# Performance work log

Hardware: AMD Instinct MI355X
Metric: run time of the kernel (lower is better)

The kernel has to match this reference:

```python
import jax, jax.numpy as jnp
import numpy as np

EMB_DIM = 1024
N_HEADS = 16  # per-head feature size after the module's axis-swapped split
D_HEAD = EMB_DIM // N_HEADS  # 64, acts as the number of attention groups
BATCH = 2
SEQ = 1024


def setup_inputs() -> dict:
    key = jax.random.key(0)
    ks = jax.random.split(key, 5)
    s = 0.02
    return {
        "x": jax.random.normal(ks[0], (BATCH, SEQ, EMB_DIM), dtype=jnp.float32),
        "Wq": jax.random.normal(ks[1], (EMB_DIM, EMB_DIM), dtype=jnp.float32) * s,
        "Wk": jax.random.normal(ks[2], (EMB_DIM, EMB_DIM), dtype=jnp.float32) * s,
        "Wv": jax.random.normal(ks[3], (EMB_DIM, EMB_DIM), dtype=jnp.float32) * s,
        "Wo": jax.random.normal(ks[4], (EMB_DIM, EMB_DIM), dtype=jnp.float32) * s,
        "bo": jnp.zeros((EMB_DIM,), dtype=jnp.float32),
    }


def reference(x, Wq, Wk, Wv, Wo, bo):
    b, n, d = x.shape
    q = x @ Wq  # [b, n, d]
    k = x @ Wk
    v = x @ Wv

    # Faithful to original split(): view (b, n, d_head, n_heads) then swap -> (b, d_head, n, n_heads)
    def split(t):
        return t.reshape(b, n, D_HEAD, N_HEADS).transpose(0, 2, 1, 3)

    q, k, v = split(q), split(k), split(v)  # [b, D_HEAD, n, N_HEADS]

    scores = jnp.einsum("bhqe,bhke->bhqk", q, k)  # [b, D_HEAD, n, n]
    causal = jnp.triu(jnp.ones((n, n), dtype=bool), k=1)
    scores = jnp.where(causal, -jnp.inf, scores)
    # Original scales by sqrt(q.shape[-1]) == sqrt(N_HEADS)
    attn = jax.nn.softmax(scores / jnp.sqrt(jnp.float32(N_HEADS)), axis=-1)
    # dropout p=0.0 (eval) -> identity
    ctx = jnp.einsum("bhqk,bhke->bhqe", attn, v)  # [b, D_HEAD, n, N_HEADS]
    ctx = ctx.transpose(0, 2, 1, 3).reshape(b, n, d)  # [b, n, emb_dim]
    return ctx @ Wo + bo
```

## Files before the change

### kernel.cpp

```cpp
#include <hip/hip_runtime.h>
#include <hip/hip_bf16.h>
#include <stdint.h>

typedef __bf16 bf16;
typedef __attribute__((ext_vector_type(8))) __bf16 bf16x8;
typedef __attribute__((ext_vector_type(4))) __bf16 bf16x4;
typedef __attribute__((ext_vector_type(2))) __bf16 bf16x2;
typedef __attribute__((ext_vector_type(4))) float f32x4;
typedef __attribute__((ext_vector_type(16))) float f32x16;
typedef __attribute__((ext_vector_type(4))) uint32_t u32x4;
typedef __attribute__((ext_vector_type(2))) uint32_t u32x2;

#define CSL 0.36067376022224085f

__device__ __forceinline__ f32x4 mfma_16x16x32(bf16x8 a, bf16x8 b, f32x4 c) {
    return __builtin_amdgcn_mfma_f32_16x16x32_bf16(a, b, c, 0, 0, 0);
}
__device__ __forceinline__ f32x16 mfma_32x32x16(bf16x8 a, bf16x8 b, f32x16 c) {
    return __builtin_amdgcn_mfma_f32_32x32x16_bf16(a, b, c, 0, 0, 0);
}

__device__ __forceinline__ void gload_lds16(const void* g, void* l) {
    __builtin_amdgcn_global_load_lds((const __attribute__((address_space(1))) uint32_t*)g,
                                     (__attribute__((address_space(3))) uint32_t*)l, 16, 0, 0);
}

__device__ __forceinline__ uint32_t cvtpk_bf16(float lo, float hi) {
    uint32_t r;
    asm("v_cvt_pk_bf16_f32 %0, %1, %2" : "=v"(r) : "v"(lo), "v"(hi));
    return r;
}
__device__ __forceinline__ u32x2 pl32(uint32_t a, uint32_t b) {
    return __builtin_amdgcn_permlane32_swap(a, b, false, false);
}
__device__ __forceinline__ bf16x8 mk_frag(uint32_t a, uint32_t b, uint32_t c, uint32_t d) {
    u32x4 t; t[0] = a; t[1] = b; t[2] = c; t[3] = d;
    return __builtin_bit_cast(bf16x8, t);
}

__global__ __launch_bounds__(256) void convert_x(const float* __restrict__ x,
                                                 bf16* __restrict__ xb) {
    const int i = blockIdx.x * 256 + threadIdx.x;
    const float4 v = ((const float4*)x)[i];
    bf16x4 o;
    o[0] = (bf16)v.x; o[1] = (bf16)v.y; o[2] = (bf16)v.z; o[3] = (bf16)v.w;
    ((bf16x4*)xb)[i] = o;
}

__global__ __launch_bounds__(256) void transcvt(const float* __restrict__ w0,
                                                const float* __restrict__ w1,
                                                const float* __restrict__ w2,
                                                const float* __restrict__ w3,
                                                bf16* __restrict__ o0,
                                                bf16* __restrict__ o1,
                                                bf16* __restrict__ o2,
                                                bf16* __restrict__ o3) {
    __shared__ float t[32][33];
    const float* src;
    bf16* dst;
    switch (blockIdx.z) {
        case 0: src = w0; dst = o0; break;
        case 1: src = w1; dst = o1; break;
        case 2: src = w2; dst = o2; break;
        default: src = w3; dst = o3; break;
    }
    const int tx = threadIdx.x, ty = threadIdx.y;
    const int bx = blockIdx.x * 32, by = blockIdx.y * 32;
#pragma unroll
    for (int i = 0; i < 4; ++i)
        t[ty + i * 8][tx] = src[(size_t)(by + ty + i * 8) * 1024 + bx + tx];
    __syncthreads();
#pragma unroll
    for (int i = 0; i < 4; ++i)
        dst[(size_t)(bx + ty + i * 8) * 1024 + by + tx] = (bf16)t[tx][ty + i * 8];
}

template<int NCOLS, int OUTF32>
__global__ __launch_bounds__(256) void gemm_bt(const bf16* __restrict__ A,
                                               const bf16* __restrict__ Bt,
                                               void* __restrict__ Cout,
                                               const float* __restrict__ bias) {
    __shared__ __align__(16) bf16 As[4096];
    __shared__ __align__(16) bf16 Bs[4096];
    const int tid = threadIdx.x;
    const int l = tid & 63, w = tid >> 6;
    const int hi = l >> 4, lo = l & 15;
    const int wr = w >> 1, wc = w & 1;
    const int brow = blockIdx.y * 128;
    const int bcol = blockIdx.x * 128;

    f32x4 acc[4][4] = {};

    for (int ks = 0; ks < 32; ++ks) {
        __syncthreads();
#pragma unroll
        for (int rnd = 0; rnd < 2; ++rnd) {
            const int u = tid + rnd * 256;
            const int kc = u >> 7, row = u & 127;
            gload_lds16(A  + (size_t)(brow + row) * 1024 + ks * 32 + kc * 8, As + u * 8);
            gload_lds16(Bt + (size_t)(bcol + row) * 1024 + ks * 32 + kc * 8, Bs + u * 8);
        }
        __syncthreads();
        bf16x8 af[4], bfr[4];
#pragma unroll
        for (int m = 0; m < 4; ++m)
            af[m] = *(const bf16x8*)(As + (hi * 128 + wr * 64 + m * 16 + lo) * 8);
#pragma unroll
        for (int n = 0; n < 4; ++n)
            bfr[n] = *(const bf16x8*)(Bs + (hi * 128 + wc * 64 + n * 16 + lo) * 8);
#pragma unroll
        for (int m = 0; m < 4; ++m)
#pragma unroll
            for (int n = 0; n < 4; ++n)
                acc[m][n] = mfma_16x16x32(af[m], bfr[n], acc[m][n]);
    }

#pragma unroll
    for (int m = 0; m < 4; ++m) {
        const int row0 = brow + wr * 64 + m * 16 + hi * 4;
#pragma unroll
        for (int n = 0; n < 4; ++n) {
            const int col = bcol + wc * 64 + n * 16 + lo;
            if (OUTF32) {
                float* C = (float*)Cout;
                const float bv = bias[col];
#pragma unroll
                for (int r = 0; r < 4; ++r)
                    C[(size_t)(row0 + r) * NCOLS + col] = acc[m][n][r] + bv;
            } else {
                bf16* C = (bf16*)Cout;
#pragma unroll
                for (int r = 0; r < 4; ++r)
                    C[(size_t)(row0 + r) * NCOLS + col] = (bf16)acc[m][n][r];
            }
        }
    }
}

__global__ __launch_bounds__(256) void attn_kernel(const bf16* __restrict__ qkv,
                                                   bf16* __restrict__ ctx) {
    __shared__ __align__(16) bf16 VT[16][1032];
    __shared__ __align__(16) bf16 KS[1024 * 16];
    const int h = blockIdx.y, bb = blockIdx.z;
    const int tid = threadIdx.x;
    const int w = tid >> 6, l = tid & 63;
    const int l5 = l & 31, hi2 = l >> 5;
    const bf16* base = qkv + (size_t)bb * 1024 * 3072;

#pragma unroll
    for (int it = 0; it < 4; ++it) {
        const int kv = it * 256 + tid;
        const bf16* vp = base + (size_t)kv * 3072 + 2048 + h * 16;
        bf16x8 v0 = *(const bf16x8*)(vp);
        bf16x8 v1 = *(const bf16x8*)(vp + 8);
#pragma unroll
        for (int e = 0; e < 8; ++e) { VT[e][kv] = v0[e]; VT[e + 8][kv] = v1[e]; }
        const bf16* kp = base + (size_t)kv * 3072 + 1024 + h * 16;
        bf16x8 k0 = *(const bf16x8*)(kp);
        bf16x8 k1 = *(const bf16x8*)(kp + 8);
        const int swz = ((kv >> 2) & 1) << 4;
        char* krow = (char*)KS + kv * 32;
        *(bf16x8*)(krow + (0 ^ swz))  = k0;
        *(bf16x8*)(krow + (16 ^ swz)) = k1;
    }
    __syncthreads();

    const int p = blockIdx.x * 4 + w;
    const int qts[2] = {p, 31 - p};

#pragma unroll 1
    for (int t = 0; t < 2; ++t) {
        const int qt = qts[t];
        const int qg = qt * 32 + l5;

        const bf16x8 qf = *(const bf16x8*)(base + (size_t)qg * 3072 + h * 16 + hi2 * 8);

        f32x16 accA = {}, accB = {};
        const f32x16 zero = {};
        float s_own = 0.0f;

        const int kv0 = l5;
        bf16x8 kf = *(const bf16x8*)((const char*)KS + kv0 * 32 +
                                     ((hi2 << 4) ^ (((kv0 >> 2) & 1) << 4)));
        bf16x8 v1f = *(const bf16x8*)(&VT[l & 15][hi2 * 8]);
        bf16x8 v2f = *(const bf16x8*)(&VT[l & 15][16 + hi2 * 8]);

        for (int kt = 0; kt <= qt; ++kt) {
            const bf16x8 kfc = kf, v1c = v1f, v2c = v2f;
            if (kt < qt) {
                const int kvn = (kt + 1) * 32 + l5;
                kf  = *(const bf16x8*)((const char*)KS + kvn * 32 +
                                       ((hi2 << 4) ^ (((kvn >> 2) & 1) << 4)));
                v1f = *(const bf16x8*)(&VT[l & 15][(kt + 1) * 32 + hi2 * 8]);
                v2f = *(const bf16x8*)(&VT[l & 15][(kt + 1) * 32 + 16 + hi2 * 8]);
            }
            const f32x16 st = mfma_32x32x16(kfc, qf, zero);

            f32x16 pr;
            if (kt < qt) {
#pragma unroll
                for (int r = 0; r < 16; ++r) pr[r] = exp2f(st[r] * CSL);
            } else {
                const int lim = qg - kt * 32;
#pragma unroll
                for (int r = 0; r < 16; ++r) {
                    const int kvr = (r & 3) + 8 * (r >> 2) + 4 * hi2;
                    pr[r] = (kvr <= lim) ? exp2f(st[r] * CSL) : 0.0f;
                }
            }
            const float b0 = (pr[0] + pr[1]) + (pr[2] + pr[3]);
            const float b1 = (pr[4] + pr[5]) + (pr[6] + pr[7]);
            const float b2 = (pr[8] + pr[9]) + (pr[10] + pr[11]);
            const float b3 = (pr[12] + pr[13]) + (pr[14] + pr[15]);
            s_own += (b0 + b1) + (b2 + b3);

            const uint32_t wa1 = cvtpk_bf16(pr[0], pr[1]), wb1 = cvtpk_bf16(pr[2], pr[3]);
            const uint32_t wc1 = cvtpk_bf16(pr[4], pr[5]), wd1 = cvtpk_bf16(pr[6], pr[7]);
            const u32x2 sA = pl32(wa1, wc1), sB = pl32(wb1, wd1);
            const bf16x8 pf1 = mk_frag(sA.x, sB.x, sA.y, sB.y);
            const uint32_t wa2 = cvtpk_bf16(pr[8], pr[9]),   wb2 = cvtpk_bf16(pr[10], pr[11]);
            const uint32_t wc2 = cvtpk_bf16(pr[12], pr[13]), wd2 = cvtpk_bf16(pr[14], pr[15]);
            const u32x2 sC = pl32(wa2, wc2), sD = pl32(wb2, wd2);
            const bf16x8 pf2 = mk_frag(sC.x, sD.x, sC.y, sD.y);

            accA = mfma_32x32x16(v1c, pf1, accA);
            accB = mfma_32x32x16(v2c, pf2, accB);
        }

        float s_tot;
        {
            const u32x2 sw = pl32(__float_as_uint(s_own), __float_as_uint(s_own));
            s_tot = __uint_as_float(sw.x) + __uint_as_float(sw.y);
        }
        const float inv = 1.0f / s_tot;
        float o[8];
#pragma unroll
        for (int r = 0; r < 8; ++r) o[r] = (accA[r] + accB[r]) * inv;
        bf16* op = ctx + ((size_t)bb * 1024 + qg) * 1024 + h * 16 + 4 * hi2;
        bf16x2 o01; o01[0] = (bf16)o[0]; o01[1] = (bf16)o[1];
        bf16x2 o23; o23[0] = (bf16)o[2]; o23[1] = (bf16)o[3];
        bf16x2 o45; o45[0] = (bf16)o[4]; o45[1] = (bf16)o[5];
        bf16x2 o67; o67[0] = (bf16)o[6]; o67[1] = (bf16)o[7];
        *(bf16x2*)(op)      = o01;
        *(bf16x2*)(op + 2)  = o23;
        *(bf16x2*)(op + 8)  = o45;
        *(bf16x2*)(op + 10) = o67;
    }
}

extern "C" void kernel_launch(void* const* d_in, const int* in_sizes, int n_in,
                              void* d_out, int out_size, void* d_ws, size_t ws_size,
                              hipStream_t stream) {
    const float* x  = (const float*)d_in[0];
    const float* Wq = (const float*)d_in[1];
    const float* Wk = (const float*)d_in[2];
    const float* Wv = (const float*)d_in[3];
    const float* Wo = (const float*)d_in[4];
    const float* bo = (const float*)d_in[5];

    char* ws = (char*)d_ws;
    bf16* xb   = (bf16*)(ws);
    bf16* wt   = (bf16*)(ws + (4  << 20));
    bf16* wot  = (bf16*)(ws + (10 << 20));
    bf16* qkv  = (bf16*)(ws + (12 << 20));
    bf16* ctx  = xb;

    convert_x<<<2048, 256, 0, stream>>>(x, xb);
    transcvt<<<dim3(32, 32, 4), dim3(32, 8), 0, stream>>>(
        Wq, Wk, Wv, Wo, wt, wt + (1 << 20), wt + (2 << 20), wot);
    gemm_bt<3072, 0><<<dim3(24, 16), 256, 0, stream>>>(xb, wt, (void*)qkv, nullptr);
    attn_kernel<<<dim3(4, 64, 2), 256, 0, stream>>>(qkv, ctx);
    gemm_bt<1024, 1><<<dim3(8, 16), 256, 0, stream>>>(ctx, wot, d_out, bo);
}
```

Measured before the change: 189.7 us.

## Split attention KV range across wave pairs, fold row sums into MFMA, shrink GEMM tiles

```diff
diff --git a/kernel.cpp b/kernel.cpp
--- a/kernel.cpp
+++ b/kernel.cpp
@@ -75,52 +75,61 @@
         dst[(size_t)(bx + ty + i * 8) * 1024 + by + tx] = (bf16)t[tx][ty + i * 8];
 }
 
-template<int NCOLS, int OUTF32>
+template<int BM, int BN, int WR, int WC, int NCOLS, int OUTF32>
 __global__ __launch_bounds__(256) void gemm_bt(const bf16* __restrict__ A,
                                                const bf16* __restrict__ Bt,
                                                void* __restrict__ Cout,
                                                const float* __restrict__ bias) {
-    __shared__ __align__(16) bf16 As[4096];
-    __shared__ __align__(16) bf16 Bs[4096];
+    constexpr int MF = BM / WR / 16;
+    constexpr int NF = BN / WC / 16;
+    constexpr int AU = BM * 4;
+    constexpr int ROUNDS = (BM + BN) / 64;
+    __shared__ __align__(16) bf16 As[BM * 32];
+    __shared__ __align__(16) bf16 Bs[BN * 32];
     const int tid = threadIdx.x;
     const int l = tid & 63, w = tid >> 6;
     const int hi = l >> 4, lo = l & 15;
-    const int wr = w >> 1, wc = w & 1;
-    const int brow = blockIdx.y * 128;
-    const int bcol = blockIdx.x * 128;
-
-    f32x4 acc[4][4] = {};
+    const int wr = w / WC, wc = w % WC;
+    const int brow = blockIdx.y * BM;
+    const int bcol = blockIdx.x * BN;
+
+    f32x4 acc[MF][NF] = {};
 
     for (int ks = 0; ks < 32; ++ks) {
         __syncthreads();
 #pragma unroll
-        for (int rnd = 0; rnd < 2; ++rnd) {
-            const int u = tid + rnd * 256;
-            const int kc = u >> 7, row = u & 127;
-            gload_lds16(A  + (size_t)(brow + row) * 1024 + ks * 32 + kc * 8, As + u * 8);
-            gload_lds16(Bt + (size_t)(bcol + row) * 1024 + ks * 32 + kc * 8, Bs + u * 8);
-        }
-        __syncthreads();
-        bf16x8 af[4], bfr[4];
-#pragma unroll
-        for (int m = 0; m < 4; ++m)
-            af[m] = *(const bf16x8*)(As + (hi * 128 + wr * 64 + m * 16 + lo) * 8);
-#pragma unroll
-        for (int n = 0; n < 4; ++n)
-            bfr[n] = *(const bf16x8*)(Bs + (hi * 128 + wc * 64 + n * 16 + lo) * 8);
-#pragma unroll
-        for (int m = 0; m < 4; ++m)
-#pragma unroll
-            for (int n = 0; n < 4; ++n)
+        for (int rnd = 0; rnd < ROUNDS; ++rnd) {
+            const int u = rnd * 256 + tid;
+            if (u < AU) {
+                const int kc = u / BM, row = u % BM;
+                gload_lds16(A + (size_t)(brow + row) * 1024 + ks * 32 + kc * 8, As + u * 8);
+            } else {
+                const int v = u - AU;
+                const int kc = v / BN, row = v % BN;
+                gload_lds16(Bt + (size_t)(bcol + row) * 1024 + ks * 32 + kc * 8, Bs + v * 8);
+            }
+        }
+        __syncthreads();
+        bf16x8 af[MF], bfr[NF];
+#pragma unroll
+        for (int m = 0; m < MF; ++m)
+            af[m] = *(const bf16x8*)(As + (hi * BM + wr * (BM / WR) + m * 16 + lo) * 8);
+#pragma unroll
+        for (int n = 0; n < NF; ++n)
+            bfr[n] = *(const bf16x8*)(Bs + (hi * BN + wc * (BN / WC) + n * 16 + lo) * 8);
+#pragma unroll
+        for (int m = 0; m < MF; ++m)
+#pragma unroll
+            for (int n = 0; n < NF; ++n)
                 acc[m][n] = mfma_16x16x32(af[m], bfr[n], acc[m][n]);
     }
 
 #pragma unroll
-    for (int m = 0; m < 4; ++m) {
-        const int row0 = brow + wr * 64 + m * 16 + hi * 4;
-#pragma unroll
-        for (int n = 0; n < 4; ++n) {
-            const int col = bcol + wc * 64 + n * 16 + lo;
+    for (int m = 0; m < MF; ++m) {
+        const int row0 = brow + wr * (BM / WR) + m * 16 + hi * 4;
+#pragma unroll
+        for (int n = 0; n < NF; ++n) {
+            const int col = bcol + wc * (BN / WC) + n * 16 + lo;
             if (OUTF32) {
                 float* C = (float*)Cout;
                 const float bv = bias[col];
@@ -137,10 +146,10 @@
     }
 }
 
-__global__ __launch_bounds__(256) void attn_kernel(const bf16* __restrict__ qkv,
-                                                   bf16* __restrict__ ctx) {
+__global__ __launch_bounds__(256, 4) void attn_kernel(const bf16* __restrict__ qkv,
+                                                      bf16* __restrict__ ctx) {
     __shared__ __align__(16) bf16 VT[16][1032];
-    __shared__ __align__(16) bf16 KS[1024 * 16];
+    __shared__ float MRG[2][64][9];
     const int h = blockIdx.y, bb = blockIdx.z;
     const int tid = threadIdx.x;
     const int w = tid >> 6, l = tid & 63;
@@ -155,64 +164,48 @@
         bf16x8 v1 = *(const bf16x8*)(vp + 8);
 #pragma unroll
         for (int e = 0; e < 8; ++e) { VT[e][kv] = v0[e]; VT[e + 8][kv] = v1[e]; }
-        const bf16* kp = base + (size_t)kv * 3072 + 1024 + h * 16;
-        bf16x8 k0 = *(const bf16x8*)(kp);
-        bf16x8 k1 = *(const bf16x8*)(kp + 8);
-        const int swz = ((kv >> 2) & 1) << 4;
-        char* krow = (char*)KS + kv * 32;
-        *(bf16x8*)(krow + (0 ^ swz))  = k0;
-        *(bf16x8*)(krow + (16 ^ swz)) = k1;
     }
     __syncthreads();
 
-    const int p = blockIdx.x * 4 + w;
+    const int pl = w >> 1, zeta = w & 1;
+    const int p = blockIdx.x * 2 + pl;
     const int qts[2] = {p, 31 - p};
+
+    bf16x8 ones;
+#pragma unroll
+    for (int i = 0; i < 8; ++i) ones[i] = (bf16)1.0f;
+    const bool isOnes = (l5 == 16) || (l5 == 20);
 
 #pragma unroll 1
     for (int t = 0; t < 2; ++t) {
         const int qt = qts[t];
+        const int S = qt + 1, H = (S + 1) >> 1;
+        const int lo_kt = zeta ? H : 0;
+        const int hi_kt = zeta ? S : H;
         const int qg = qt * 32 + l5;
 
         const bf16x8 qf = *(const bf16x8*)(base + (size_t)qg * 3072 + h * 16 + hi2 * 8);
 
         f32x16 accA = {}, accB = {};
         const f32x16 zero = {};
-        float s_own = 0.0f;
-
-        const int kv0 = l5;
-        bf16x8 kf = *(const bf16x8*)((const char*)KS + kv0 * 32 +
-                                     ((hi2 << 4) ^ (((kv0 >> 2) & 1) << 4)));
-        bf16x8 v1f = *(const bf16x8*)(&VT[l & 15][hi2 * 8]);
-        bf16x8 v2f = *(const bf16x8*)(&VT[l & 15][16 + hi2 * 8]);
-
-        for (int kt = 0; kt <= qt; ++kt) {
-            const bf16x8 kfc = kf, v1c = v1f, v2c = v2f;
-            if (kt < qt) {
-                const int kvn = (kt + 1) * 32 + l5;
-                kf  = *(const bf16x8*)((const char*)KS + kvn * 32 +
-                                       ((hi2 << 4) ^ (((kvn >> 2) & 1) << 4)));
-                v1f = *(const bf16x8*)(&VT[l & 15][(kt + 1) * 32 + hi2 * 8]);
-                v2f = *(const bf16x8*)(&VT[l & 15][(kt + 1) * 32 + 16 + hi2 * 8]);
-            }
-            const f32x16 st = mfma_32x32x16(kfc, qf, zero);
+
+#pragma unroll 1
+        for (int kt = lo_kt; kt < hi_kt; ++kt) {
+            const bf16x8 kf = *(const bf16x8*)(base + (size_t)(kt * 32 + l5) * 3072 + 1024 + h * 16 + hi2 * 8);
+            const f32x16 st = mfma_32x32x16(kf, qf, zero);
 
             f32x16 pr;
-            if (kt < qt) {
-#pragma unroll
-                for (int r = 0; r < 16; ++r) pr[r] = exp2f(st[r] * CSL);
-            } else {
-                const int lim = qg - kt * 32;
+            if (kt == qt) {
+                const int lim = l5;
 #pragma unroll
                 for (int r = 0; r < 16; ++r) {
                     const int kvr = (r & 3) + 8 * (r >> 2) + 4 * hi2;
                     pr[r] = (kvr <= lim) ? exp2f(st[r] * CSL) : 0.0f;
                 }
+            } else {
+#pragma unroll
+                for (int r = 0; r < 16; ++r) pr[r] = exp2f(st[r] * CSL);
             }
-            const float b0 = (pr[0] + pr[1]) + (pr[2] + pr[3]);
-            const float b1 = (pr[4] + pr[5]) + (pr[6] + pr[7]);
-            const float b2 = (pr[8] + pr[9]) + (pr[10] + pr[11]);
-            const float b3 = (pr[12] + pr[13]) + (pr[14] + pr[15]);
-            s_own += (b0 + b1) + (b2 + b3);
 
             const uint32_t wa1 = cvtpk_bf16(pr[0], pr[1]), wb1 = cvtpk_bf16(pr[2], pr[3]);
             const uint32_t wc1 = cvtpk_bf16(pr[4], pr[5]), wd1 = cvtpk_bf16(pr[6], pr[7]);
@@ -223,28 +216,38 @@
             const u32x2 sC = pl32(wa2, wc2), sD = pl32(wb2, wd2);
             const bf16x8 pf2 = mk_frag(sC.x, sD.x, sC.y, sD.y);
 
-            accA = mfma_32x32x16(v1c, pf1, accA);
-            accB = mfma_32x32x16(v2c, pf2, accB);
-        }
-
-        float s_tot;
-        {
-            const u32x2 sw = pl32(__float_as_uint(s_own), __float_as_uint(s_own));
-            s_tot = __uint_as_float(sw.x) + __uint_as_float(sw.y);
-        }
-        const float inv = 1.0f / s_tot;
-        float o[8];
-#pragma unroll
-        for (int r = 0; r < 8; ++r) o[r] = (accA[r] + accB[r]) * inv;
-        bf16* op = ctx + ((size_t)bb * 1024 + qg) * 1024 + h * 16 + 4 * hi2;
-        bf16x2 o01; o01[0] = (bf16)o[0]; o01[1] = (bf16)o[1];
-        bf16x2 o23; o23[0] = (bf16)o[2]; o23[1] = (bf16)o[3];
-        bf16x2 o45; o45[0] = (bf16)o[4]; o45[1] = (bf16)o[5];
-        bf16x2 o67; o67[0] = (bf16)o[6]; o67[1] = (bf16)o[7];
-        *(bf16x2*)(op)      = o01;
-        *(bf16x2*)(op + 2)  = o23;
-        *(bf16x2*)(op + 8)  = o45;
-        *(bf16x2*)(op + 10) = o67;
+            const bf16* va = &VT[l & 15][kt * 32 + hi2 * 8];
+            bf16x8 vf1 = *(const bf16x8*)va;
+            bf16x8 vf2 = *(const bf16x8*)(va + 16);
+            if (isOnes) { vf1 = ones; vf2 = ones; }
+            accA = mfma_32x32x16(vf1, pf1, accA);
+            accB = mfma_32x32x16(vf2, pf2, accB);
+        }
+
+        float part[9];
+#pragma unroll
+        for (int i = 0; i < 9; ++i) part[i] = accA[i] + accB[i];
+
+        if (zeta) {
+#pragma unroll
+            for (int i = 0; i < 9; ++i) MRG[pl][l][i] = part[i];
+        }
+        __syncthreads();
+        if (!zeta) {
+#pragma unroll
+            for (int i = 0; i < 9; ++i) part[i] += MRG[pl][l][i];
+            const float inv = 1.0f / part[8];
+            bf16* op = ctx + ((size_t)bb * 1024 + qg) * 1024 + h * 16 + 4 * hi2;
+            bf16x2 o01; o01[0] = (bf16)(part[0] * inv); o01[1] = (bf16)(part[1] * inv);
+            bf16x2 o23; o23[0] = (bf16)(part[2] * inv); o23[1] = (bf16)(part[3] * inv);
+            bf16x2 o45; o45[0] = (bf16)(part[4] * inv); o45[1] = (bf16)(part[5] * inv);
+            bf16x2 o67; o67[0] = (bf16)(part[6] * inv); o67[1] = (bf16)(part[7] * inv);
+            *(bf16x2*)(op)      = o01;
+            *(bf16x2*)(op + 2)  = o23;
+            *(bf16x2*)(op + 8)  = o45;
+            *(bf16x2*)(op + 10) = o67;
+        }
+        __syncthreads();
     }
 }
 
@@ -268,7 +271,7 @@
     convert_x<<<2048, 256, 0, stream>>>(x, xb);
     transcvt<<<dim3(32, 32, 4), dim3(32, 8), 0, stream>>>(
         Wq, Wk, Wv, Wo, wt, wt + (1 << 20), wt + (2 << 20), wot);
-    gemm_bt<3072, 0><<<dim3(24, 16), 256, 0, stream>>>(xb, wt, (void*)qkv, nullptr);
-    attn_kernel<<<dim3(4, 64, 2), 256, 0, stream>>>(qkv, ctx);
-    gemm_bt<1024, 1><<<dim3(8, 16), 256, 0, stream>>>(ctx, wot, d_out, bo);
-}
+    gemm_bt<64, 128, 2, 2, 3072, 0><<<dim3(24, 32), 256, 0, stream>>>(xb, wt, (void*)qkv, nullptr);
+    attn_kernel<<<dim3(8, 64, 2), 256, 0, stream>>>(qkv, ctx);
+    gemm_bt<64, 64, 2, 2, 1024, 1><<<dim3(16, 32), 256, 0, stream>>>(ctx, wot, d_out, bo);
+}
```

Result: faster. 173.5 us (-8.5%).
